# Kernel tuning notes

Measured on AMD Instinct MI355X. Metric: run time of the kernel, lower is better.

The kernel has to match this reference:

```python
import jax, jax.numpy as jnp
import numpy as np

CUTOFF_FREQ = 4000.0
SAMPLE_RATE = 48000.0
FILTER_ORDER = 6


def _butter_lowpass(order, wn):
    """Digital Butterworth low-pass (b, a), matching scipy.signal.butter(order, wn, 'low')."""
    fs = 2.0
    warped = 2.0 * fs * np.tan(np.pi * wn / fs)
    # Analog Butterworth prototype poles (buttap)
    m = np.arange(-order + 1, order, 2)
    p = -np.exp(1j * np.pi * m / (2 * order))
    k = 1.0
    # lp2lp: scale poles by warped cutoff
    p = warped * p
    k = k * warped ** order
    # Bilinear transform (fs=2); zeros map to -1
    fs2 = 2.0 * fs
    pz = (fs2 + p) / (fs2 - p)
    kz = k * np.real(1.0 / np.prod(fs2 - p))
    zz = -np.ones(order)
    b = (kz * np.poly(zz)).real
    a = np.poly(pz).real
    return b.astype(np.float32), a.astype(np.float32)

_B, _A = _butter_lowpass(FILTER_ORDER, CUTOFF_FREQ / (0.5 * SAMPLE_RATE))


def _lfilter(x):
    """IIR filter along last axis, direct-form II transposed (matches scipy.signal.lfilter
    with zero initial state). x: [B, T] -> [B, T]."""
    b = jnp.asarray(_B, x.dtype)
    a = jnp.asarray(_A, x.dtype)
    n = b.shape[0] - 1  # filter order
    b0, bi, ai = b[0], b[1:], a[1:]

    def step(z, x_t):  # z: [B, n], x_t: [B]
        y = b0 * x_t + z[:, 0]
        z_shift = jnp.concatenate([z[:, 1:], jnp.zeros_like(z[:, :1])], axis=1)
        z_new = z_shift + bi[None, :] * x_t[:, None] - ai[None, :] * y[:, None]
        return z_new, y

    z0 = jnp.zeros((x.shape[0], n), x.dtype)
    _, ys = jax.lax.scan(step, z0, x.T)  # ys: [T, B]
    return ys.T


def setup_inputs() -> dict:
    key = jax.random.key(0)
    k1, k2 = jax.random.split(key)
    B, T = 96, 131072
    output = jax.random.normal(k1, (B, T), dtype=jnp.float32)
    target = jax.random.normal(k2, (B, T), dtype=jnp.float32)
    return {"output": output, "target": target}


def reference(output, target):
    filtered_output = _lfilter(output)
    filtered_target = _lfilter(target)
    return jnp.mean(jnp.abs(filtered_output - filtered_target))
```

## Files before the change

### kernel.cpp

```cpp
#include <hip/hip_runtime.h>
#include <cmath>
#include <complex>

#define T_LEN   131072
#define B_ROWS  96
#define CHUNK   16
#define WARM    64
#define SEG     4096
#define NSEG    (T_LEN / SEG)
#define NLDS    (SEG + WARM)
#define NF4     (NLDS / 4)
#define BLOCK   256
#define WPT     20
#define GRID    (B_ROWS * NSEG)
#define RNDS    17

struct Coefs {
  float b0, b1, b2, b3, b4, b5, b6;
  float a1, a2, a3, a4, a5, a6;
  float invN;
};

__device__ __forceinline__ int swz(int f) { return f ^ ((f >> 3) & 7); }

#define GLDS(gp, lp)                                                        \
  __builtin_amdgcn_global_load_lds(                                         \
      (const __attribute__((address_space(1))) void*)(gp),                  \
      (__attribute__((address_space(3))) void*)(lp), 16, 0, 0)

#define LP_STEP(x, ACC)                                  \
  {                                                      \
    float y = fmaf(cf.b0, (x), z0);                      \
    ACC;                                                 \
    z0 = fmaf(-cf.a1, y, fmaf(cf.b1, (x), z1));          \
    z1 = fmaf(-cf.a2, y, fmaf(cf.b2, (x), z2));          \
    z2 = fmaf(-cf.a3, y, fmaf(cf.b3, (x), z3));          \
    z3 = fmaf(-cf.a4, y, fmaf(cf.b4, (x), z4));          \
    z4 = fmaf(-cf.a5, y, fmaf(cf.b5, (x), z5));          \
    z5 = fmaf(-cf.a6, y, cf.b6 * (x));                   \
  }

__global__ __launch_bounds__(BLOCK, 4) void lp_mae_kernel(
    const float* __restrict__ out_p, const float* __restrict__ tgt_p,
    const float4* __restrict__ zbuf,
    float* __restrict__ partial, Coefs cf)
{
  __shared__ float4 ldsA[NF4];
  __shared__ float4 ldsB[NF4];
  __shared__ float red[BLOCK / 64];

  const int lane = threadIdx.x & 63;
  const int wv   = threadIdx.x >> 6;
  const int blk  = blockIdx.x;
  const int row  = blk >> 5;
  const int s    = blk & (NSEG - 1);
  const bool first = (s == 0);

  const size_t segbase = (size_t)row * T_LEN + (size_t)s * SEG;
  const float4* po = (const float4*)(out_p + segbase - WARM);
  const float4* pt = (const float4*)(tgt_p + segbase - WARM);

  for (int r = wv; r < RNDS; r += 4) {
    const int g = r * 64 + lane;
    if (g < NF4) {
      const float4* ga = po + swz(g);
      const float4* gb = pt + swz(g);
      if (first && r == 0 && lane < (WARM / 4)) {
        ga = zbuf + lane;
        gb = zbuf + lane;
      }
      GLDS(ga, ldsA + r * 64);
      GLDS(gb, ldsB + r * 64);
    }
  }
  __syncthreads();

  float4 w[WPT];
  #pragma unroll
  for (int j = 0; j < WPT; ++j) {
    const int idx = swz(threadIdx.x * 4 + j);
    float4 a = ldsA[idx];
    float4 b = ldsB[idx];
    w[j] = make_float4(a.x - b.x, a.y - b.y, a.z - b.z, a.w - b.w);
  }

  float z0 = 0.f, z1 = 0.f, z2 = 0.f, z3 = 0.f, z4 = 0.f, z5 = 0.f;
  float sum = 0.f;

  #pragma unroll
  for (int j = 0; j < WARM / 4; ++j) {
    LP_STEP(w[j].x, );
    LP_STEP(w[j].y, );
    LP_STEP(w[j].z, );
    LP_STEP(w[j].w, );
  }
  #pragma unroll
  for (int j = WARM / 4; j < WPT; ++j) {
    LP_STEP(w[j].x, sum += fabsf(y));
    LP_STEP(w[j].y, sum += fabsf(y));
    LP_STEP(w[j].z, sum += fabsf(y));
    LP_STEP(w[j].w, sum += fabsf(y));
  }

  #pragma unroll
  for (int off = 32; off > 0; off >>= 1)
    sum += __shfl_down(sum, off);
  if (lane == 0)
    red[wv] = sum;
  __syncthreads();
  if (threadIdx.x == 0)
    partial[blk] = red[0] + red[1] + red[2] + red[3];
}

__global__ __launch_bounds__(BLOCK) void lp_reduce_kernel(
    const float* __restrict__ partial, float* __restrict__ dout, float invN)
{
  __shared__ float red[BLOCK / 64];
  float sum = 0.f;
  for (int i = threadIdx.x; i < GRID; i += BLOCK)
    sum += partial[i];
  #pragma unroll
  for (int off = 32; off > 0; off >>= 1)
    sum += __shfl_down(sum, off);
  if ((threadIdx.x & 63) == 0)
    red[threadIdx.x >> 6] = sum;
  __syncthreads();
  if (threadIdx.x == 0)
    dout[0] = (red[0] + red[1] + red[2] + red[3]) * invN;
}

extern "C" void kernel_launch(void* const* d_in, const int* in_sizes, int n_in,
                              void* d_out, int out_size, void* d_ws, size_t ws_size,
                              hipStream_t stream) {
  (void)in_sizes; (void)n_in; (void)ws_size; (void)out_size;

  const float* out_p = (const float*)d_in[0];
  const float* tgt_p = (const float*)d_in[1];
  float* dout = (float*)d_out;
  float* partial = (float*)d_ws;
  float4* zbuf = (float4*)((char*)d_ws + 16384);

  using cd = std::complex<double>;
  const int order = 6;
  const double wn = 4000.0 / 24000.0;
  const double fs = 2.0;
  const double warped = 2.0 * fs * std::tan(M_PI * wn / fs);

  cd p[6];
  for (int k = 0; k < order; ++k) {
    int m = -order + 1 + 2 * k;
    p[k] = -std::exp(cd(0.0, M_PI * m / (2.0 * order))) * warped;
  }
  double kgain = std::pow(warped, (double)order);
  const double fs2 = 2.0 * fs;

  cd pz[6];
  cd prodden(1.0, 0.0);
  for (int k = 0; k < order; ++k) {
    pz[k] = (fs2 + p[k]) / (fs2 - p[k]);
    prodden *= (fs2 - p[k]);
  }
  double kz = kgain * std::real(1.0 / prodden);

  const double binom[7] = {1, 6, 15, 20, 15, 6, 1};
  double bd[7];
  for (int i = 0; i < 7; ++i) bd[i] = kz * binom[i];

  cd ac[7];
  ac[0] = cd(1.0, 0.0);
  for (int i = 1; i < 7; ++i) ac[i] = cd(0.0, 0.0);
  for (int k = 0; k < order; ++k)
    for (int i = k + 1; i >= 1; --i)
      ac[i] = ac[i] - pz[k] * ac[i - 1];

  Coefs cf;
  cf.b0 = (float)bd[0]; cf.b1 = (float)bd[1]; cf.b2 = (float)bd[2];
  cf.b3 = (float)bd[3]; cf.b4 = (float)bd[4]; cf.b5 = (float)bd[5];
  cf.b6 = (float)bd[6];
  cf.a1 = (float)std::real(ac[1]); cf.a2 = (float)std::real(ac[2]);
  cf.a3 = (float)std::real(ac[3]); cf.a4 = (float)std::real(ac[4]);
  cf.a5 = (float)std::real(ac[5]); cf.a6 = (float)std::real(ac[6]);
  cf.invN = 1.0f / (float)((double)B_ROWS * (double)T_LEN);

  hipMemsetAsync(zbuf, 0, 16 * sizeof(float4), stream);
  lp_mae_kernel<<<GRID, BLOCK, 0, stream>>>(out_p, tgt_p, zbuf, partial, cf);
  lp_reduce_kernel<<<1, BLOCK, 0, stream>>>(partial, dout, cf.invN);
}
```

Baseline: 130.9 us.

## Pipeline per-wave double-buffered segment loads with persistent waves and shorter warmup

Restructures the filter kernel so each wave owns six 1024-sample segments and double-buffers their global-to-LDS loads, waiting with a vmcnt threshold instead of block-wide barriers. The grid shrinks to a fixed 512 blocks and partial sums are written per wave. The IIR warm-up is reduced from 64 to 48 samples, which cuts redundant recurrence work but slightly loosens how closely the truncated state matches the exact filter. This is meant to hide memory latency behind compute and remove synchronisation, at the cost of more dynamic LDS per block and lower occupancy.

```diff
diff --git a/kernel.cpp b/kernel.cpp
--- a/kernel.cpp
+++ b/kernel.cpp
@@ -5,15 +5,17 @@
 #define T_LEN   131072
 #define B_ROWS  96
 #define CHUNK   16
-#define WARM    64
-#define SEG     4096
-#define NSEG    (T_LEN / SEG)
-#define NLDS    (SEG + WARM)
-#define NF4     (NLDS / 4)
+#define WARM    48
+#define WSEG    1024
+#define SSTG    268
+#define PSTG    272
+#define SEGROW  128
+#define NWAVE   2048
+#define SPW     6
 #define BLOCK   256
-#define WPT     20
-#define GRID    (B_ROWS * NSEG)
-#define RNDS    17
+#define GRIDN   512
+#define PREFN   10
+#define LDSBYTES (4 * 2 * 2 * PSTG * 16)
 
 struct Coefs {
   float b0, b1, b2, b3, b4, b5, b6;
@@ -27,6 +29,8 @@
   __builtin_amdgcn_global_load_lds(                                         \
       (const __attribute__((address_space(1))) void*)(gp),                  \
       (__attribute__((address_space(3))) void*)(lp), 16, 0, 0)
+
+#define WAITCNT_VM(N) __builtin_amdgcn_s_waitcnt(0x0F70 | (N))
 
 #define LP_STEP(x, ACC)                                  \
   {                                                      \
@@ -40,76 +44,93 @@
     z5 = fmaf(-cf.a6, y, cf.b6 * (x));                   \
   }
 
-__global__ __launch_bounds__(BLOCK, 4) void lp_mae_kernel(
+__device__ __forceinline__ void issue_seg(
+    const float* __restrict__ out_p, const float* __restrict__ tgt_p,
+    const float4* __restrict__ zbuf, float4* slice, int lane, int g, int b)
+{
+  const int row = g >> 7;
+  const int s   = g & (SEGROW - 1);
+  const size_t segbase = (size_t)row * T_LEN + (size_t)s * WSEG;
+  const float4* po = (const float4*)(out_p + segbase) - (WARM / 4);
+  const float4* pt = (const float4*)(tgt_p + segbase) - (WARM / 4);
+  const bool first = (s == 0);
+
+  float4* la = slice + (b * 2 + 0) * PSTG;
+  float4* lb = slice + (b * 2 + 1) * PSTG;
+
+  #pragma unroll
+  for (int r = 0; r < 4; ++r) {
+    const int q = r * 64 + lane;
+    const float4* ga = po + swz(q);
+    const float4* gb = pt + swz(q);
+    if (first && q < (WARM / 4)) {
+      ga = zbuf + lane;
+      gb = zbuf + lane;
+    }
+    GLDS(ga, la + r * 64);
+    GLDS(gb, lb + r * 64);
+  }
+  if (lane < (SSTG - 256)) {
+    const int q = 256 + lane;
+    GLDS(po + swz(q), la + 256);
+    GLDS(pt + swz(q), lb + 256);
+  }
+}
+
+__global__ __launch_bounds__(BLOCK, 2) void lp_mae_kernel(
     const float* __restrict__ out_p, const float* __restrict__ tgt_p,
     const float4* __restrict__ zbuf,
     float* __restrict__ partial, Coefs cf)
 {
-  __shared__ float4 ldsA[NF4];
-  __shared__ float4 ldsB[NF4];
-  __shared__ float red[BLOCK / 64];
+  extern __shared__ float4 xsall[];
 
   const int lane = threadIdx.x & 63;
   const int wv   = threadIdx.x >> 6;
-  const int blk  = blockIdx.x;
-  const int row  = blk >> 5;
-  const int s    = blk & (NSEG - 1);
-  const bool first = (s == 0);
-
-  const size_t segbase = (size_t)row * T_LEN + (size_t)s * SEG;
-  const float4* po = (const float4*)(out_p + segbase - WARM);
-  const float4* pt = (const float4*)(tgt_p + segbase - WARM);
-
-  for (int r = wv; r < RNDS; r += 4) {
-    const int g = r * 64 + lane;
-    if (g < NF4) {
-      const float4* ga = po + swz(g);
-      const float4* gb = pt + swz(g);
-      if (first && r == 0 && lane < (WARM / 4)) {
-        ga = zbuf + lane;
-        gb = zbuf + lane;
+  const int wid  = blockIdx.x * 4 + wv;
+  float4* slice  = xsall + wv * (2 * 2 * PSTG);
+
+  float sum = 0.f;
+
+  issue_seg(out_p, tgt_p, zbuf, slice, lane, wid * SPW, 0);
+
+  #pragma unroll
+  for (int k = 0; k < SPW; ++k) {
+    const int b = k & 1;
+    if (k + 1 < SPW)
+      issue_seg(out_p, tgt_p, zbuf, slice, lane, wid * SPW + k + 1, b ^ 1);
+
+    if (k + 1 < SPW) WAITCNT_VM(PREFN);
+    else             WAITCNT_VM(0);
+
+    const float4* la = slice + (b * 2 + 0) * PSTG;
+    const float4* lb = slice + (b * 2 + 1) * PSTG;
+    const int base = lane * 4;
+
+    float z0 = 0.f, z1 = 0.f, z2 = 0.f, z3 = 0.f, z4 = 0.f, z5 = 0.f;
+    #pragma unroll
+    for (int j = 0; j < 16; ++j) {
+      const int idx = swz(base + j);
+      const float4 a = la[idx];
+      const float4 t = lb[idx];
+      if (j < WARM / 4) {
+        LP_STEP(a.x - t.x, );
+        LP_STEP(a.y - t.y, );
+        LP_STEP(a.z - t.z, );
+        LP_STEP(a.w - t.w, );
+      } else {
+        LP_STEP(a.x - t.x, sum += fabsf(y));
+        LP_STEP(a.y - t.y, sum += fabsf(y));
+        LP_STEP(a.z - t.z, sum += fabsf(y));
+        LP_STEP(a.w - t.w, sum += fabsf(y));
       }
-      GLDS(ga, ldsA + r * 64);
-      GLDS(gb, ldsB + r * 64);
     }
-  }
-  __syncthreads();
-
-  float4 w[WPT];
-  #pragma unroll
-  for (int j = 0; j < WPT; ++j) {
-    const int idx = swz(threadIdx.x * 4 + j);
-    float4 a = ldsA[idx];
-    float4 b = ldsB[idx];
-    w[j] = make_float4(a.x - b.x, a.y - b.y, a.z - b.z, a.w - b.w);
-  }
-
-  float z0 = 0.f, z1 = 0.f, z2 = 0.f, z3 = 0.f, z4 = 0.f, z5 = 0.f;
-  float sum = 0.f;
-
-  #pragma unroll
-  for (int j = 0; j < WARM / 4; ++j) {
-    LP_STEP(w[j].x, );
-    LP_STEP(w[j].y, );
-    LP_STEP(w[j].z, );
-    LP_STEP(w[j].w, );
-  }
-  #pragma unroll
-  for (int j = WARM / 4; j < WPT; ++j) {
-    LP_STEP(w[j].x, sum += fabsf(y));
-    LP_STEP(w[j].y, sum += fabsf(y));
-    LP_STEP(w[j].z, sum += fabsf(y));
-    LP_STEP(w[j].w, sum += fabsf(y));
   }
 
   #pragma unroll
   for (int off = 32; off > 0; off >>= 1)
     sum += __shfl_down(sum, off);
   if (lane == 0)
-    red[wv] = sum;
-  __syncthreads();
-  if (threadIdx.x == 0)
-    partial[blk] = red[0] + red[1] + red[2] + red[3];
+    partial[wid] = sum;
 }
 
 __global__ __launch_bounds__(BLOCK) void lp_reduce_kernel(
@@ -117,7 +138,7 @@
 {
   __shared__ float red[BLOCK / 64];
   float sum = 0.f;
-  for (int i = threadIdx.x; i < GRID; i += BLOCK)
+  for (int i = threadIdx.x; i < NWAVE; i += BLOCK)
     sum += partial[i];
   #pragma unroll
   for (int off = 32; off > 0; off >>= 1)
@@ -138,7 +159,7 @@
   const float* tgt_p = (const float*)d_in[1];
   float* dout = (float*)d_out;
   float* partial = (float*)d_ws;
-  float4* zbuf = (float4*)((char*)d_ws + 16384);
+  float4* zbuf = (float4*)((char*)d_ws + 32768);
 
   using cd = std::complex<double>;
   const int order = 6;
@@ -183,6 +204,6 @@
   cf.invN = 1.0f / (float)((double)B_ROWS * (double)T_LEN);
 
   hipMemsetAsync(zbuf, 0, 16 * sizeof(float4), stream);
-  lp_mae_kernel<<<GRID, BLOCK, 0, stream>>>(out_p, tgt_p, zbuf, partial, cf);
+  lp_mae_kernel<<<GRIDN, BLOCK, LDSBYTES, stream>>>(out_p, tgt_p, zbuf, partial, cf);
   lp_reduce_kernel<<<1, BLOCK, 0, stream>>>(partial, dout, cf.invN);
 }
```

After: 211.5 us. 61.6% more time.
